# Kernel tuning notes

Measured on AMD Instinct MI355X. Metric: run time of the kernel, lower is better.

The kernel has to match this reference:

```python
import jax, jax.numpy as jnp
import numpy as np

HIDDEN = 1152
N_HEADS = 4
N_KV = 1
HEAD_DIM = 256
EPS = 1e-6
B, S = 4, 2048
ROPE_THETA = 1000000.0


def _rms_norm(x, w):
    # x: [..., D] float32; Gemma-style (1 + w) scale
    xf = x.astype(jnp.float32)
    inv = jax.lax.rsqrt(jnp.mean(xf * xf, axis=-1, keepdims=True) + EPS)
    return (xf * inv * (1.0 + w.astype(jnp.float32))).astype(x.dtype)


def _apply_rope(x, cos, sin):
    # x: [B, H, S, D]; cos/sin: [S, D/2]
    d2 = x.shape[-1] // 2
    x1, x2 = x[..., :d2], x[..., d2:]
    cos = cos[None, None, :, :]
    sin = sin[None, None, :, :]
    xr = x1 * cos - x2 * sin
    xi = x1 * sin + x2 * cos
    return jnp.concatenate([xr, xi], axis=-1).astype(x.dtype)


def setup_inputs() -> dict:
    key = jax.random.key(0)
    k_h, k_qkv, k_qn, k_kn, k_o = jax.random.split(key, 5)
    hidden_states = jax.random.normal(k_h, (B, S, HIDDEN), dtype=jnp.float32)
    # causal additive mask [1,1,S,S]
    neg = jnp.finfo(jnp.float32).min
    causal = jnp.tril(jnp.ones((S, S), dtype=bool))
    attention_mask = jnp.where(causal, 0.0, neg)[None, None, :, :].astype(jnp.float32)
    # RoPE tables (complex freqs_cis split into cos/sin)
    inv_freq = 1.0 / (ROPE_THETA ** (np.arange(0, HEAD_DIM, 2, dtype=np.float32) / HEAD_DIM))
    ang = np.arange(S, dtype=np.float32)[:, None] * inv_freq[None, :]
    freqs_cos = jnp.asarray(np.cos(ang))
    freqs_sin = jnp.asarray(np.sin(ang))
    qkv_out = (N_HEADS + 2 * N_KV) * HEAD_DIM
    scale = HIDDEN ** -0.5
    w_qkv = jax.random.normal(k_qkv, (HIDDEN, qkv_out), dtype=jnp.float32) * scale
    w_o = jax.random.normal(k_o, (N_HEADS * HEAD_DIM, HIDDEN), dtype=jnp.float32) * (N_HEADS * HEAD_DIM) ** -0.5
    q_norm_w = jax.random.normal(k_qn, (HEAD_DIM,), dtype=jnp.float32) * 0.02
    k_norm_w = jax.random.normal(k_kn, (HEAD_DIM,), dtype=jnp.float32) * 0.02
    return {
        "hidden_states": hidden_states,
        "attention_mask": attention_mask,
        "freqs_cos": freqs_cos,
        "freqs_sin": freqs_sin,
        "w_qkv": w_qkv,
        "q_norm_w": q_norm_w,
        "k_norm_w": k_norm_w,
        "w_o": w_o,
    }


def reference(hidden_states, attention_mask, freqs_cos, freqs_sin, w_qkv, q_norm_w, k_norm_w, w_o):
    b, s, _ = hidden_states.shape
    groups = N_HEADS // N_KV
    scaling = HEAD_DIM ** -0.5

    qkv = jnp.einsum("bsh,ho->bso", hidden_states, w_qkv)
    q_end = N_HEADS * HEAD_DIM
    k_end = q_end + N_KV * HEAD_DIM
    q = qkv[:, :, :q_end].reshape(b, s, N_HEADS, HEAD_DIM).transpose(0, 2, 1, 3)
    k = qkv[:, :, q_end:k_end].reshape(b, s, N_KV, HEAD_DIM).transpose(0, 2, 1, 3)
    v = qkv[:, :, k_end:].reshape(b, s, N_KV, HEAD_DIM).transpose(0, 2, 1, 3)

    q = _rms_norm(q, q_norm_w)
    k = _rms_norm(k, k_norm_w)

    q = _apply_rope(q, freqs_cos, freqs_sin)
    k = _apply_rope(k, freqs_cos, freqs_sin)

    if groups > 1:
        k = jnp.repeat(k, groups, axis=1)  # [B, H, S, D]
        v = jnp.repeat(v, groups, axis=1)

    scores = jnp.einsum("bhqd,bhkd->bhqk", q * scaling, k)
    scores = scores + attention_mask.astype(jnp.float32)
    probs = jax.nn.softmax(scores.astype(jnp.float32), axis=-1).astype(q.dtype)

    attn = jnp.einsum("bhqk,bhkd->bhqd", probs, v)
    attn = attn.transpose(0, 2, 1, 3).reshape(b, s, N_HEADS * HEAD_DIM)
    return jnp.einsum("bsf,fh->bsh", attn, w_o)
```

## Files before the change

### kernel.cpp

```cpp
#include <hip/hip_runtime.h>

typedef _Float16 f16;
typedef _Float16 f16x8 __attribute__((ext_vector_type(8)));
typedef _Float16 f16x4 __attribute__((ext_vector_type(4)));
typedef float f32x4 __attribute__((ext_vector_type(4)));

#define NH 4
#define HD 256
#define BB 4
#define SS 2048
#define HID 1152
#define QKV_N 1536
#define ODIM (NH * HD)

__global__ __launch_bounds__(256) void transpose_cvt(
    const float* __restrict__ src, long src_ld, long src_bs,
    f16* __restrict__ dst, long dst_ld, long dst_bs) {
  __shared__ float tile[32][33];
  src += (long)blockIdx.z * src_bs;
  dst += (long)blockIdx.z * dst_bs;
  int r0 = blockIdx.y * 32, c0 = blockIdx.x * 32;
  int tc = threadIdx.x & 31, tr = threadIdx.x >> 5;
#pragma unroll
  for (int i = 0; i < 4; ++i)
    tile[tr + i * 8][tc] = src[(long)(r0 + tr + i * 8) * src_ld + c0 + tc];
  __syncthreads();
#pragma unroll
  for (int i = 0; i < 4; ++i)
    dst[(long)(c0 + tr + i * 8) * dst_ld + r0 + tc] = (f16)tile[tc][tr + i * 8];
}

__global__ __launch_bounds__(256, 2) void gemm_a32_b16(
    const float* __restrict__ A, const f16* __restrict__ Bt,
    float* __restrict__ C, int K, int N) {
  __shared__ f16 As[128][40];
  __shared__ f16 Bs[128][40];
  int tid = threadIdx.x;
  int wave = tid >> 6, lane = tid & 63;
  int l16 = lane & 15, lhi = lane >> 4;
  int wm = (wave >> 1) * 64, wn = (wave & 1) * 64;
  long bm = (long)blockIdx.x * 128, bn = (long)blockIdx.y * 128;
  f32x4 acc[4][4] = {};
  int a_kq = (tid & 7) * 4, a_r = tid >> 3;
  int b_ko = (tid & 3) * 8, b_r = tid >> 2;

  for (int k0 = 0; k0 < K; k0 += 32) {
#pragma unroll
    for (int i = 0; i < 4; ++i) {
      int r = a_r + 32 * i;
      float4 v = *(const float4*)&A[(bm + r) * K + k0 + a_kq];
      f16x4 h = {(f16)v.x, (f16)v.y, (f16)v.z, (f16)v.w};
      *(f16x4*)&As[r][a_kq] = h;
    }
#pragma unroll
    for (int i = 0; i < 2; ++i) {
      int r = b_r + 64 * i;
      *(uint4*)&Bs[r][b_ko] = *(const uint4*)&Bt[(bn + r) * K + k0 + b_ko];
    }
    __syncthreads();
    f16x8 af[4], bf[4];
#pragma unroll
    for (int i = 0; i < 4; ++i)
      af[i] = *(const f16x8*)&As[wm + i * 16 + l16][lhi * 8];
#pragma unroll
    for (int j = 0; j < 4; ++j)
      bf[j] = *(const f16x8*)&Bs[wn + j * 16 + l16][lhi * 8];
#pragma unroll
    for (int i = 0; i < 4; ++i)
#pragma unroll
      for (int j = 0; j < 4; ++j)
        acc[i][j] = __builtin_amdgcn_mfma_f32_16x16x32_f16(af[i], bf[j], acc[i][j], 0, 0, 0);
    __syncthreads();
  }
#pragma unroll
  for (int i = 0; i < 4; ++i) {
    long row = bm + wm + i * 16 + lhi * 4;
#pragma unroll
    for (int r = 0; r < 4; ++r) {
      float* crow = C + (row + r) * N + bn + wn + l16;
#pragma unroll
      for (int j = 0; j < 4; ++j) crow[j * 16] = acc[i][j][r];
    }
  }
}

__device__ __forceinline__ void norm_rope_store(
    const float* __restrict__ x, const float* __restrict__ w,
    const float* __restrict__ fc, const float* __restrict__ fs,
    f16* __restrict__ dst, float scale, int lane) {
  float x0 = x[lane], x1 = x[lane + 64], x2 = x[lane + 128], x3 = x[lane + 192];
  float ss = x0 * x0 + x1 * x1 + x2 * x2 + x3 * x3;
#pragma unroll
  for (int m = 1; m < 64; m <<= 1) ss += __shfl_xor(ss, m, 64);
  float inv = rsqrtf(ss * (1.0f / 256.0f) + 1e-6f);
  x0 *= inv * (1.0f + w[lane]);
  x1 *= inv * (1.0f + w[lane + 64]);
  x2 *= inv * (1.0f + w[lane + 128]);
  x3 *= inv * (1.0f + w[lane + 192]);
  float c0 = fc[lane], s0 = fs[lane], c1 = fc[lane + 64], s1 = fs[lane + 64];
  dst[lane]       = (f16)((x0 * c0 - x2 * s0) * scale);
  dst[lane + 64]  = (f16)((x1 * c1 - x3 * s1) * scale);
  dst[lane + 128] = (f16)((x0 * s0 + x2 * c0) * scale);
  dst[lane + 192] = (f16)((x1 * s1 + x3 * c1) * scale);
}

__global__ __launch_bounds__(256) void qkv_post(
    const float* __restrict__ qkv, const float* __restrict__ qnw,
    const float* __restrict__ knw, const float* __restrict__ fcos,
    const float* __restrict__ fsin, f16* __restrict__ Q, f16* __restrict__ Kb) {
  long row = blockIdx.x;
  int b = (int)(row >> 11), s = (int)(row & 2047);
  int wave = threadIdx.x >> 6, lane = threadIdx.x & 63;
  const float* base = qkv + row * QKV_N;
  const float* fc = fcos + (long)s * 128;
  const float* fs = fsin + (long)s * 128;
  norm_rope_store(base + wave * HD, qnw, fc, fs,
                  Q + ((long)(b * NH + wave) * SS + s) * HD, 0.0625f, lane);
  if (wave == 0)
    norm_rope_store(base + NH * HD, knw, fc, fs, Kb + row * HD, 1.0f, lane);
}

__global__ __launch_bounds__(256, 2) void attn_fwd(
    const f16* __restrict__ Q, const f16* __restrict__ Kb,
    const f16* __restrict__ Vt, float* __restrict__ O) {
  __shared__ f16 Klds[32][264];
  __shared__ f16 Vlds[256][40];
  __shared__ f16 Plds[4][16][40];
  int qb = blockIdx.x, h = blockIdx.y, b = blockIdx.z;
  int tid = threadIdx.x, wave = tid >> 6, lane = tid & 63;
  int l16 = lane & 15, lhi = lane >> 4;
  int q0 = qb * 64 + wave * 16;

  f16x8 qf[8];
  const f16* Qbase = Q + ((long)(b * NH + h) * SS + q0 + l16) * HD + lhi * 8;
#pragma unroll
  for (int kb = 0; kb < 8; ++kb) qf[kb] = *(const f16x8*)(Qbase + kb * 32);

  f32x4 o[16] = {};
  float m_i[4] = {-1e30f, -1e30f, -1e30f, -1e30f};
  float l_i[4] = {0.f, 0.f, 0.f, 0.f};
  const f16* Kg = Kb + (long)b * SS * HD;
  const f16* Vg = Vt + (long)b * HD * SS;
  int ntiles = qb * 2 + 2;

  for (int t = 0; t < ntiles; ++t) {
    int kv0 = t * 32;
    __syncthreads();
    {
      int c8 = (tid & 31) * 8, r = tid >> 5;
#pragma unroll
      for (int i = 0; i < 4; ++i)
        *(uint4*)&Klds[r + i * 8][c8] =
            *(const uint4*)(Kg + (long)(kv0 + r + i * 8) * HD + c8);
      int c8v = (tid & 3) * 8, rv = tid >> 2;
#pragma unroll
      for (int i = 0; i < 4; ++i)
        *(uint4*)&Vlds[rv + i * 64][c8v] =
            *(const uint4*)(Vg + (long)(rv + i * 64) * SS + kv0 + c8v);
    }
    __syncthreads();

    f32x4 sc[2] = {};
#pragma unroll
    for (int kb = 0; kb < 8; ++kb) {
#pragma unroll
      for (int cf = 0; cf < 2; ++cf) {
        f16x8 bf = *(const f16x8*)&Klds[cf * 16 + l16][kb * 32 + lhi * 8];
        sc[cf] = __builtin_amdgcn_mfma_f32_16x16x32_f16(qf[kb], bf, sc[cf], 0, 0, 0);
      }
    }

    float p0[4], p1[4], scl[4];
#pragma unroll
    for (int r = 0; r < 4; ++r) {
      int q = q0 + lhi * 4 + r;
      float s0 = (kv0 + l16 <= q) ? sc[0][r] : -1e30f;
      float s1 = (kv0 + 16 + l16 <= q) ? sc[1][r] : -1e30f;
      float mx = fmaxf(s0, s1);
      mx = fmaxf(mx, __shfl_xor(mx, 1));
      mx = fmaxf(mx, __shfl_xor(mx, 2));
      mx = fmaxf(mx, __shfl_xor(mx, 4));
      mx = fmaxf(mx, __shfl_xor(mx, 8));
      float mn = fmaxf(m_i[r], mx);
      float sc_ = __expf(m_i[r] - mn);
      p0[r] = __expf(s0 - mn);
      p1[r] = __expf(s1 - mn);
      float rs = p0[r] + p1[r];
      rs += __shfl_xor(rs, 1);
      rs += __shfl_xor(rs, 2);
      rs += __shfl_xor(rs, 4);
      rs += __shfl_xor(rs, 8);
      l_i[r] = l_i[r] * sc_ + rs;
      m_i[r] = mn;
      scl[r] = sc_;
    }
#pragma unroll
    for (int nf = 0; nf < 16; ++nf)
#pragma unroll
      for (int r = 0; r < 4; ++r) o[nf][r] *= scl[r];

#pragma unroll
    for (int r = 0; r < 4; ++r) {
      Plds[wave][lhi * 4 + r][l16] = (f16)p0[r];
      Plds[wave][lhi * 4 + r][16 + l16] = (f16)p1[r];
    }
    asm volatile("s_waitcnt lgkmcnt(0)" ::: "memory");
    f16x8 pa = *(const f16x8*)&Plds[wave][l16][lhi * 8];
#pragma unroll
    for (int nf = 0; nf < 16; ++nf) {
      f16x8 vf = *(const f16x8*)&Vlds[nf * 16 + l16][lhi * 8];
      o[nf] = __builtin_amdgcn_mfma_f32_16x16x32_f16(pa, vf, o[nf], 0, 0, 0);
    }
  }

#pragma unroll
  for (int r = 0; r < 4; ++r) {
    float invl = 1.0f / l_i[r];
    long srow = q0 + lhi * 4 + r;
    float* Orow = O + ((long)b * SS + srow) * ODIM + h * HD + l16;
#pragma unroll
    for (int nf = 0; nf < 16; ++nf) Orow[nf * 16] = o[nf][r] * invl;
  }
}

extern "C" void kernel_launch(void* const* d_in, const int* in_sizes, int n_in,
                              void* d_out, int out_size, void* d_ws, size_t ws_size,
                              hipStream_t stream) {
  const float* hidden = (const float*)d_in[0];
  const float* fcos = (const float*)d_in[2];
  const float* fsin = (const float*)d_in[3];
  const float* wqkv = (const float*)d_in[4];
  const float* qnw = (const float*)d_in[5];
  const float* knw = (const float*)d_in[6];
  const float* wo = (const float*)d_in[7];
  float* out = (float*)d_out;

  char* ws = (char*)d_ws;
  float* qkv = (float*)(ws + 0);
  float* Obuf = (float*)(ws + 0);
  f16* Qb = (f16*)(ws + 50331648);
  f16* Kb = (f16*)(ws + 67108864);
  f16* Vt = (f16*)(ws + 71303168);
  f16* wqkvt = (f16*)(ws + 75497472);
  f16* wot = (f16*)(ws + 79036416);

  transpose_cvt<<<dim3(QKV_N / 32, HID / 32, 1), 256, 0, stream>>>(
      wqkv, QKV_N, 0, wqkvt, HID, 0);
  transpose_cvt<<<dim3(HID / 32, ODIM / 32, 1), 256, 0, stream>>>(
      wo, HID, 0, wot, ODIM, 0);

  gemm_a32_b16<<<dim3(BB * SS / 128, QKV_N / 128), 256, 0, stream>>>(
      hidden, wqkvt, qkv, HID, QKV_N);

  qkv_post<<<dim3(BB * SS), 256, 0, stream>>>(qkv, qnw, knw, fcos, fsin, Qb, Kb);

  transpose_cvt<<<dim3(HD / 32, SS / 32, BB), 256, 0, stream>>>(
      qkv + 1280, QKV_N, (long)SS * QKV_N, Vt, SS, (long)HD * SS);

  attn_fwd<<<dim3(SS / 64, NH, BB), 256, 0, stream>>>(Qb, Kb, Vt, Obuf);

  gemm_a32_b16<<<dim3(BB * SS / 128, HID / 128), 256, 0, stream>>>(
      Obuf, wot, out, ODIM, HID);
}
```

Before: 272.9 us.

## Restructure attention: 64-wide KV tiles, register prefetch, transposed QK, reversed block order

The attention kernel now processes 64 keys per tile instead of 32, prefetching the next K/V tile into registers while computing the current one. QK^T is computed transposed (K as A operand), so each lane holds one query row and the softmax reductions need only two cross-lane shuffles, and the causal mask is applied only on the diagonal tile. Query blocks are launched in reverse order so the longest causal blocks start first. The prefetch registers and larger LDS raise register and shared-memory pressure, which may reduce occupancy under the 2-blocks-per-CU bound.

```diff
diff --git a/kernel.cpp b/kernel.cpp
--- a/kernel.cpp
+++ b/kernel.cpp
@@ -123,103 +123,149 @@
 __global__ __launch_bounds__(256, 2) void attn_fwd(
     const f16* __restrict__ Q, const f16* __restrict__ Kb,
     const f16* __restrict__ Vt, float* __restrict__ O) {
-  __shared__ f16 Klds[32][264];
-  __shared__ f16 Vlds[256][40];
-  __shared__ f16 Plds[4][16][40];
-  int qb = blockIdx.x, h = blockIdx.y, b = blockIdx.z;
+  __shared__ f16 Klds[64][264];
+  __shared__ f16 Vlds[256][72];
+  __shared__ f16 Plds[4][16][72];
+  int qb = 31 - blockIdx.x;
+  int h = blockIdx.y, b = blockIdx.z;
   int tid = threadIdx.x, wave = tid >> 6, lane = tid & 63;
   int l16 = lane & 15, lhi = lane >> 4;
   int q0 = qb * 64 + wave * 16;
 
+  const f16* Kg = Kb + (long)b * SS * HD;
+  const f16* Vg = Vt + (long)b * HD * SS;
+
   f16x8 qf[8];
   const f16* Qbase = Q + ((long)(b * NH + h) * SS + q0 + l16) * HD + lhi * 8;
 #pragma unroll
   for (int kb = 0; kb < 8; ++kb) qf[kb] = *(const f16x8*)(Qbase + kb * 32);
 
   f32x4 o[16] = {};
-  float m_i[4] = {-1e30f, -1e30f, -1e30f, -1e30f};
-  float l_i[4] = {0.f, 0.f, 0.f, 0.f};
-  const f16* Kg = Kb + (long)b * SS * HD;
-  const f16* Vg = Vt + (long)b * HD * SS;
-  int ntiles = qb * 2 + 2;
-
-  for (int t = 0; t < ntiles; ++t) {
-    int kv0 = t * 32;
+  float m_i = -1e30f, l_i = 0.f;
+
+  int krow = tid >> 5, kcol = (tid & 31) * 8;
+  int vrow = tid >> 3, vcol = (tid & 7) * 8;
+  uint4 kreg[8], vreg[8];
+  int nt = qb + 1;
+
+  {
+    const f16* kp = Kg + (long)krow * HD + kcol;
+    const f16* vp = Vg + (long)vrow * SS + vcol;
+#pragma unroll
+    for (int i = 0; i < 8; ++i) kreg[i] = *(const uint4*)(kp + (long)i * 8 * HD);
+#pragma unroll
+    for (int i = 0; i < 8; ++i) vreg[i] = *(const uint4*)(vp + (long)i * 32 * SS);
+  }
+
+  for (int t = 0; t < nt; ++t) {
     __syncthreads();
-    {
-      int c8 = (tid & 31) * 8, r = tid >> 5;
-#pragma unroll
-      for (int i = 0; i < 4; ++i)
-        *(uint4*)&Klds[r + i * 8][c8] =
-            *(const uint4*)(Kg + (long)(kv0 + r + i * 8) * HD + c8);
-      int c8v = (tid & 3) * 8, rv = tid >> 2;
-#pragma unroll
-      for (int i = 0; i < 4; ++i)
-        *(uint4*)&Vlds[rv + i * 64][c8v] =
-            *(const uint4*)(Vg + (long)(rv + i * 64) * SS + kv0 + c8v);
+#pragma unroll
+    for (int i = 0; i < 8; ++i) *(uint4*)&Klds[krow + i * 8][kcol] = kreg[i];
+#pragma unroll
+    for (int i = 0; i < 8; ++i) *(uint4*)&Vlds[vrow + i * 32][vcol] = vreg[i];
+    if (t + 1 < nt) {
+      long kv0n = (long)(t + 1) * 64;
+      const f16* kp = Kg + (kv0n + krow) * HD + kcol;
+      const f16* vp = Vg + (long)vrow * SS + kv0n + vcol;
+#pragma unroll
+      for (int i = 0; i < 8; ++i) kreg[i] = *(const uint4*)(kp + (long)i * 8 * HD);
+#pragma unroll
+      for (int i = 0; i < 8; ++i) vreg[i] = *(const uint4*)(vp + (long)i * 32 * SS);
     }
     __syncthreads();
 
-    f32x4 sc[2] = {};
+    int kv0 = t * 64;
+    f32x4 sc[4] = {};
 #pragma unroll
     for (int kb = 0; kb < 8; ++kb) {
 #pragma unroll
-      for (int cf = 0; cf < 2; ++cf) {
-        f16x8 bf = *(const f16x8*)&Klds[cf * 16 + l16][kb * 32 + lhi * 8];
-        sc[cf] = __builtin_amdgcn_mfma_f32_16x16x32_f16(qf[kb], bf, sc[cf], 0, 0, 0);
+      for (int cf = 0; cf < 4; ++cf) {
+        f16x8 kf = *(const f16x8*)&Klds[cf * 16 + l16][kb * 32 + lhi * 8];
+        sc[cf] = __builtin_amdgcn_mfma_f32_16x16x32_f16(kf, qf[kb], sc[cf], 0, 0, 0);
       }
     }
 
-    float p0[4], p1[4], scl[4];
-#pragma unroll
-    for (int r = 0; r < 4; ++r) {
-      int q = q0 + lhi * 4 + r;
-      float s0 = (kv0 + l16 <= q) ? sc[0][r] : -1e30f;
-      float s1 = (kv0 + 16 + l16 <= q) ? sc[1][r] : -1e30f;
-      float mx = fmaxf(s0, s1);
-      mx = fmaxf(mx, __shfl_xor(mx, 1));
-      mx = fmaxf(mx, __shfl_xor(mx, 2));
-      mx = fmaxf(mx, __shfl_xor(mx, 4));
-      mx = fmaxf(mx, __shfl_xor(mx, 8));
-      float mn = fmaxf(m_i[r], mx);
-      float sc_ = __expf(m_i[r] - mn);
-      p0[r] = __expf(s0 - mn);
-      p1[r] = __expf(s1 - mn);
-      float rs = p0[r] + p1[r];
-      rs += __shfl_xor(rs, 1);
-      rs += __shfl_xor(rs, 2);
-      rs += __shfl_xor(rs, 4);
-      rs += __shfl_xor(rs, 8);
-      l_i[r] = l_i[r] * sc_ + rs;
-      m_i[r] = mn;
-      scl[r] = sc_;
-    }
-#pragma unroll
-    for (int nf = 0; nf < 16; ++nf)
-#pragma unroll
-      for (int r = 0; r < 4; ++r) o[nf][r] *= scl[r];
-
-#pragma unroll
-    for (int r = 0; r < 4; ++r) {
-      Plds[wave][lhi * 4 + r][l16] = (f16)p0[r];
-      Plds[wave][lhi * 4 + r][16 + l16] = (f16)p1[r];
-    }
+    float p[16];
+    float mx = -1e30f;
+    int qrow = q0 + l16;
+    if (t == qb) {
+#pragma unroll
+      for (int cf = 0; cf < 4; ++cf)
+#pragma unroll
+        for (int r = 0; r < 4; ++r) {
+          int kv = kv0 + cf * 16 + lhi * 4 + r;
+          float s = (kv <= qrow) ? sc[cf][r] : -1e30f;
+          p[cf * 4 + r] = s;
+          mx = fmaxf(mx, s);
+        }
+    } else {
+#pragma unroll
+      for (int i = 0; i < 16; ++i) {
+        float s = sc[i >> 2][i & 3];
+        p[i] = s;
+        mx = fmaxf(mx, s);
+      }
+    }
+    mx = fmaxf(mx, __shfl_xor(mx, 16));
+    mx = fmaxf(mx, __shfl_xor(mx, 32));
+    float mn = fmaxf(m_i, mx);
+    float scl = __expf(m_i - mn);
+    float rs = 0.f;
+#pragma unroll
+    for (int i = 0; i < 16; ++i) {
+      p[i] = __expf(p[i] - mn);
+      rs += p[i];
+    }
+    rs += __shfl_xor(rs, 16);
+    rs += __shfl_xor(rs, 32);
+    l_i = l_i * scl + rs;
+    m_i = mn;
+
+#pragma unroll
+    for (int cf = 0; cf < 4; ++cf) {
+      f16x4 hp = {(f16)p[cf * 4], (f16)p[cf * 4 + 1], (f16)p[cf * 4 + 2],
+                  (f16)p[cf * 4 + 3]};
+      *(f16x4*)&Plds[wave][l16][cf * 16 + lhi * 4] = hp;
+    }
+
+    float s0 = __shfl(scl, lhi * 4 + 0);
+    float s1 = __shfl(scl, lhi * 4 + 1);
+    float s2 = __shfl(scl, lhi * 4 + 2);
+    float s3 = __shfl(scl, lhi * 4 + 3);
+#pragma unroll
+    for (int nf = 0; nf < 16; ++nf) {
+      o[nf][0] *= s0;
+      o[nf][1] *= s1;
+      o[nf][2] *= s2;
+      o[nf][3] *= s3;
+    }
+
     asm volatile("s_waitcnt lgkmcnt(0)" ::: "memory");
-    f16x8 pa = *(const f16x8*)&Plds[wave][l16][lhi * 8];
-#pragma unroll
-    for (int nf = 0; nf < 16; ++nf) {
-      f16x8 vf = *(const f16x8*)&Vlds[nf * 16 + l16][lhi * 8];
-      o[nf] = __builtin_amdgcn_mfma_f32_16x16x32_f16(pa, vf, o[nf], 0, 0, 0);
-    }
-  }
-
+    __builtin_amdgcn_sched_barrier(0);
+
+#pragma unroll
+    for (int ks = 0; ks < 2; ++ks) {
+      f16x8 pa = *(const f16x8*)&Plds[wave][l16][ks * 32 + lhi * 8];
+#pragma unroll
+      for (int nf = 0; nf < 16; ++nf) {
+        f16x8 vf = *(const f16x8*)&Vlds[nf * 16 + l16][ks * 32 + lhi * 8];
+        o[nf] = __builtin_amdgcn_mfma_f32_16x16x32_f16(pa, vf, o[nf], 0, 0, 0);
+      }
+    }
+  }
+
+  float inv = 1.0f / l_i;
+  float i0 = __shfl(inv, lhi * 4 + 0);
+  float i1 = __shfl(inv, lhi * 4 + 1);
+  float i2 = __shfl(inv, lhi * 4 + 2);
+  float i3 = __shfl(inv, lhi * 4 + 3);
+  float ir[4] = {i0, i1, i2, i3};
 #pragma unroll
   for (int r = 0; r < 4; ++r) {
-    float invl = 1.0f / l_i[r];
     long srow = q0 + lhi * 4 + r;
     float* Orow = O + ((long)b * SS + srow) * ODIM + h * HD + l16;
 #pragma unroll
-    for (int nf = 0; nf < 16; ++nf) Orow[nf * 16] = o[nf][r] * invl;
+    for (int nf = 0; nf < 16; ++nf) Orow[nf * 16] = o[nf][r] * ir[r];
   }
 }
 
@@ -257,7 +303,7 @@
   transpose_cvt<<<dim3(HD / 32, SS / 32, BB), 256, 0, stream>>>(
       qkv + 1280, QKV_N, (long)SS * QKV_N, Vt, SS, (long)HD * SS);
 
-  attn_fwd<<<dim3(SS / 64, NH, BB), 256, 0, stream>>>(Qb, Kb, Vt, Obuf);
+  attn_fwd<<<dim3(32, NH, BB), 256, 0, stream>>>(Qb, Kb, Vt, Obuf);
 
   gemm_a32_b16<<<dim3(BB * SS / 128, HID / 128), 256, 0, stream>>>(
       Obuf, wot, out, ODIM, HID);
```

After: 419.1 us. +53.6%, slower.
